# Performance work log

Hardware: AMD Instinct MI355X
Metric: run time of the kernel (lower is better)

## Reference

```python
import jax, jax.numpy as jnp
import numpy as np

N = 262144
BN_EPS = 1e-5


def gcn_conv(x, edge_index, edge_weight, W, b):
    """PyG GCNConv: symmetric norm with added self-loops (fill value 1).
    out[i] = sum_e d^{-1/2}[src] * w_e * d^{-1/2}[dst] * (x[src] @ W) + b
    """
    src, dst = edge_index[0], edge_index[1]
    loops = jnp.arange(N)
    src2 = jnp.concatenate([src, loops])
    dst2 = jnp.concatenate([dst, loops])
    ew2 = jnp.concatenate([edge_weight, jnp.ones((N,), edge_weight.dtype)])
    deg = jax.ops.segment_sum(ew2, dst2, num_segments=N)  # [N]
    dinv = jnp.where(deg > 0, jax.lax.rsqrt(deg), 0.0)
    norm = dinv[src2] * ew2 * dinv[dst2]  # [E+N]
    h = x @ W  # [N, out_c] tiny GEMM
    msg = h[src2] * norm[:, None]  # gather + scale, [E+N, out_c]
    out = jax.ops.segment_sum(msg, dst2, num_segments=N)  # scatter-add
    return out + b


def bn_eval(x, gamma, beta, mean, var):
    # BatchNorm1d in eval mode (running statistics)
    return (x - mean) * (gamma * jax.lax.rsqrt(var + BN_EPS)) + beta


def setup_inputs() -> dict:
    key = jax.random.key(0)
    ks = jax.random.split(key, 16)
    E = 4194304
    inp = {
        "x": jax.random.normal(ks[0], (N, 1), jnp.float32),
        "edge_index": jax.random.randint(ks[1], (2, E), 0, N, jnp.int64),
        "edge_weight": jax.random.uniform(ks[2], (E,), jnp.float32),
        # GCNConv weights (lin has no bias fused; bias added after aggregation)
        "W1": jax.random.normal(ks[3], (1, 16), jnp.float32) * 0.5,
        "b1": jnp.zeros((16,), jnp.float32),
        "W2": jax.random.normal(ks[4], (16, 4), jnp.float32) * 0.25,
        "b2": jnp.zeros((4,), jnp.float32),
        "W3": jax.random.normal(ks[5], (4, 1), jnp.float32) * 0.5,
        "b3": jnp.zeros((1,), jnp.float32),
        # BatchNorm params (eval-mode running stats)
        "g1": jnp.ones((16,), jnp.float32), "be1": jnp.zeros((16,), jnp.float32),
        "m1": jax.random.normal(ks[6], (16,), jnp.float32) * 0.1,
        "v1": jax.random.uniform(ks[7], (16,), jnp.float32, 0.5, 1.5),
        "g2": jnp.ones((4,), jnp.float32), "be2": jnp.zeros((4,), jnp.float32),
        "m2": jax.random.normal(ks[8], (4,), jnp.float32) * 0.1,
        "v2": jax.random.uniform(ks[9], (4,), jnp.float32, 0.5, 1.5),
        # final Linear
        "We": jax.random.normal(ks[10], (1, 1), jnp.float32),
        "bee": jnp.zeros((1,), jnp.float32),
    }
    return inp


def reference(x, edge_index, edge_weight, W1, b1, W2, b2, W3, b3,
              g1, be1, m1, v1, g2, be2, m2, v2, We, bee):
    h = gcn_conv(x, edge_index, edge_weight, W1, b1)
    h = jax.nn.relu(bn_eval(h, g1, be1, m1, v1))  # dropout = identity (eval)
    h = gcn_conv(h, edge_index, edge_weight, W2, b2)
    h = jax.nn.relu(bn_eval(h, g2, be2, m2, v2))
    h = gcn_conv(h, edge_index, edge_weight, W3, b3)
    h = h @ We + bee
    return jax.nn.sigmoid(h)
```

## Files before the change

kernel.cpp:

```cpp
#include <hip/hip_runtime.h>
#include <hip/hip_fp16.h>
#include <math.h>


#define BN_EPS 1e-5f
#define BKT_BITS 9
#define BKT_SZ 512
#define NBKT 512
#define PB 1024
#define PT 512
#define STAGE_CAP 4096
#define SHD 8
#define CAPS 1280
#define CAPR (SHD*CAPS)
#define CAPL 8960
#define CHUNK_R 9
#define NGRP 128
#define NBL 2048
#define CAP2 2560
#define SW(p) ((p) ^ (((p) >> 5) & 31))

__device__ inline float wdec(int e) {
    return __half2float(__ushort_as_half((unsigned short)((((unsigned)e) >> 18) << 1)));
}

__global__ void k_zero(int* __restrict__ gcur, int m) {
    int i = blockIdx.x * blockDim.x + threadIdx.x;
    if (i < m) gcur[i] = 0;
}

__device__ inline void scat1(int d, int s, int wbits, int* __restrict__ cur,
                             const int* __restrict__ basem, int2* __restrict__ stage) {
    int bk = ((unsigned)d) >> BKT_BITS;
    int dloc = d & (BKT_SZ - 1);
    int pos = atomicAdd(&cur[bk], 1);
    int dest = basem[bk] + pos;
    unsigned h = (unsigned)(__half_as_ushort(__float2half(__int_as_float(wbits))) & 0x7FFF);
    unsigned w14 = (h >> 1) + (h & 1);
    stage[pos] = make_int2(
        (int)((unsigned)s | ((unsigned)dloc << 18) | (((unsigned)dest & 31u) << 27)),
        (int)(w14 | (((unsigned)dest >> 5) << 14)));
}

__global__ __launch_bounds__(PT, 8) void k_scatter(
        const int* __restrict__ src, const int* __restrict__ dst,
        const float* __restrict__ w, int* __restrict__ gcur,
        int2* __restrict__ sorted, int E) {
    __shared__ int cur[NBKT];
    __shared__ int basem[NBKT];
    __shared__ int wsum[8];
    __shared__ int2 stage[STAGE_CAP];
    int t = threadIdx.x, b = blockIdx.x;
    cur[t] = 0;
    __syncthreads();
    int lo = b * STAGE_CAP;
    const int4* dp = (const int4*)(dst + lo);
    const int4* sp = (const int4*)(src + lo);
    const int4* wp = (const int4*)(w + lo);
    int4 d4a = dp[t];
    int4 d4b = dp[t + PT];
    int4 s4a = sp[t], s4b = sp[t + PT];
    int4 w4a = wp[t], w4b = wp[t + PT];
    atomicAdd(&cur[((unsigned)d4a.x) >> BKT_BITS], 1);
    atomicAdd(&cur[((unsigned)d4a.y) >> BKT_BITS], 1);
    atomicAdd(&cur[((unsigned)d4a.z) >> BKT_BITS], 1);
    atomicAdd(&cur[((unsigned)d4a.w) >> BKT_BITS], 1);
    atomicAdd(&cur[((unsigned)d4b.x) >> BKT_BITS], 1);
    atomicAdd(&cur[((unsigned)d4b.y) >> BKT_BITS], 1);
    atomicAdd(&cur[((unsigned)d4b.z) >> BKT_BITS], 1);
    atomicAdd(&cur[((unsigned)d4b.w) >> BKT_BITS], 1);
    __syncthreads();
    int v = cur[t];
    int lane = t & 63, wid = t >> 6;
    int inc = v;
#pragma unroll
    for (int off = 1; off < 64; off <<= 1) {
        int u = __shfl_up(inc, off);
        if (lane >= off) inc += u;
    }
    if (lane == 63) wsum[wid] = inc;
    __syncthreads();
    if (t == 0) {
        int s = 0;
#pragma unroll
        for (int i = 0; i < 8; ++i) { int c = wsum[i]; wsum[i] = s; s += c; }
    }
    __syncthreads();
    int excl = inc - v + wsum[wid];
    int shard = b & (SHD - 1);
    int gbase = v ? atomicAdd(&gcur[((t << 3) | shard) << 4], v) : 0;
    cur[t] = excl;
    basem[t] = t * CAPR + shard * CAPS + gbase - excl;
    __syncthreads();
    scat1(d4a.x, s4a.x, w4a.x, cur, basem, stage);
    scat1(d4a.y, s4a.y, w4a.y, cur, basem, stage);
    scat1(d4a.z, s4a.z, w4a.z, cur, basem, stage);
    scat1(d4a.w, s4a.w, w4a.w, cur, basem, stage);
    scat1(d4b.x, s4b.x, w4b.x, cur, basem, stage);
    scat1(d4b.y, s4b.y, w4b.y, cur, basem, stage);
    scat1(d4b.z, s4b.z, w4b.z, cur, basem, stage);
    scat1(d4b.w, s4b.w, w4b.w, cur, basem, stage);
    __syncthreads();
    for (int p = t; p < STAGE_CAP; p += PT) {
        int2 sv = stage[p];
        unsigned w0 = (unsigned)sv.x, w1 = (unsigned)sv.y;
        int dest = (int)(((w1 >> 14) << 5) | (w0 >> 27));
        sorted[dest] = make_int2((int)(w0 & 0x07FFFFFF), (int)(w1 & 0x3FFF));
    }
}

__global__ __launch_bounds__(1024, 8) void k_sortdeg(
        const int* __restrict__ gcur, int2* __restrict__ sorted,
        const float* __restrict__ x, float* __restrict__ dinv,
        float* __restrict__ xs, int* __restrict__ starts,
        int* __restrict__ gend) {
    __shared__ int lpk[CAPL];
    __shared__ int cnt[BKT_SZ];
    __shared__ int sts[BKT_SZ + 1];
    __shared__ int wsum2[8];
    __shared__ int ssh[SHD];
    __shared__ int soff[SHD + 1];
    __shared__ float degp[BKT_SZ];
    int t = threadIdx.x, b = blockIdx.x;
    if (t < BKT_SZ) cnt[t] = 0;
    if (t < SHD) ssh[t] = min(gcur[((b << 3) | t) << 4], CAPS);
    __syncthreads();
    if (t == 0) {
        int s = 0;
#pragma unroll
        for (int i = 0; i < SHD; ++i) { soff[i] = s; s += ssh[i]; }
        soff[SHD] = min(s, CAPL);
    }
    __syncthreads();
    int len = soff[SHD];
    int rbase = b * CAPR;

    int e27[CHUNK_R], wrk[CHUNK_R];
#pragma unroll
    for (int r = 0; r < CHUNK_R; ++r) {
        int k = t + (r << 10);
        if (k < len) {
            int s = 0;
#pragma unroll
            for (int q = 1; q < SHD; ++q) s += (k >= soff[q]) ? 1 : 0;
            int2 v = sorted[rbase + s * CAPS + (k - soff[s])];
            e27[r] = v.x;
            int rk = atomicAdd(&cnt[((unsigned)v.x) >> 18], 1);
            wrk[r] = (v.y & 0x3FFF) | (rk << 14);
        }
    }
    __syncthreads();
    int c_own = (t < BKT_SZ) ? cnt[t] : 0;
    int lane = t & 63, wid = t >> 6;
    int inc = c_own;
#pragma unroll
    for (int o = 1; o < 64; o <<= 1) {
        int u = __shfl_up(inc, o);
        if (lane >= o) inc += u;
    }
    if (t < BKT_SZ && lane == 63) wsum2[wid] = inc;
    __syncthreads();
    if (t == 0) {
        int s = 0;
#pragma unroll
        for (int i = 0; i < 8; ++i) { int c = wsum2[i]; wsum2[i] = s; s += c; }
    }
    __syncthreads();
    if (t < BKT_SZ) sts[t] = inc - c_own + wsum2[wid];
    if (t == 0) sts[BKT_SZ] = len;
    __syncthreads();
#pragma unroll
    for (int r = 0; r < CHUNK_R; ++r) {
        int k = t + (r << 10);
        if (k < len) {
            int e = e27[r];
            int pos = sts[((unsigned)e) >> 18] + (((unsigned)wrk[r]) >> 14);
            lpk[SW(pos)] = (e & 0x3FFFF) | ((wrk[r] & 0x3FFF) << 18);
        }
    }
    __syncthreads();

    int pbase = 2 * rbase;
    {
        int node = t & (BKT_SZ - 1);
        int jh = t >> 9;
        int c0 = sts[node], c1 = sts[node + 1];
        int half = (c1 - c0) >> 1;
        int kb = jh ? (c0 + half) : c0;
        int ke = jh ? c1 : (c0 + half);
        float s = 0.f;
        for (int k = kb; k < ke; ++k) s += wdec(lpk[SW(k)]);
        if (jh) degp[node] = s;
        __syncthreads();
        if (!jh) {
            s += degp[node];
            float di = rsqrtf(1.0f + s);
            int i = b * BKT_SZ + node;
            dinv[i] = di;
            xs[i] = di * x[i];
            starts[i] = pbase + c0;
        }
    }
    if (t < 4)
        gend[b * 4 + t] = pbase + ((t == 3) ? len : sts[(t + 1) * NGRP]);

    int* srtp = (int*)sorted;
    for (int k4 = (t << 2); k4 < len; k4 += 4096) {
        if (k4 + 3 < len) {
            int4 v;
            v.x = lpk[SW(k4)]; v.y = lpk[SW(k4 + 1)];
            v.z = lpk[SW(k4 + 2)]; v.w = lpk[SW(k4 + 3)];
            *(int4*)(srtp + pbase + k4) = v;
        } else {
            for (int k = k4; k < len; ++k) srtp[pbase + k] = lpk[SW(k)];
        }
    }
}

__global__ __launch_bounds__(512, 8) void k_l1(
        const int* __restrict__ starts, const int* __restrict__ gend,
        const int* __restrict__ srtp,
        const float* __restrict__ xs, const float* __restrict__ dinv,
        const float* __restrict__ W1, const float* __restrict__ b1,
        const float* __restrict__ g1, const float* __restrict__ be1,
        const float* __restrict__ m1, const float* __restrict__ v1,
        const float* __restrict__ W2, int2* __restrict__ hs2p) {
    __shared__ int eds[CAP2 + 32];
    __shared__ float part[3][NGRP];
    __shared__ float s1w[16], bb1[16];
    int t = threadIdx.x, b = blockIdx.x;
    int i0 = b * NGRP;
    if (t < 16) {
        float s = g1[t] * rsqrtf(v1[t] + BN_EPS);
        s1w[t] = W1[t] * s;
        bb1[t] = fmaf(b1[t] - m1[t], s, be1[t]);
    }
    int lo = starts[i0];
    int lo2 = lo & ~3;
    int len2 = min(gend[b] - lo, CAP2) + (lo - lo2);
    for (int k4 = (t << 2); k4 < len2; k4 += 2048) {
        int4 v = *(const int4*)(srtp + lo2 + k4);
        eds[SW(k4)] = v.x;
        if (k4 + 1 < len2) eds[SW(k4 + 1)] = v.y;
        if (k4 + 2 < len2) eds[SW(k4 + 2)] = v.z;
        if (k4 + 3 < len2) eds[SW(k4 + 3)] = v.w;
    }
    __syncthreads();
    int li = t & (NGRP - 1);
    int j = t >> 7;
    int i = i0 + li;
    int c0 = starts[i] - lo2;
    int c1 = (li == NGRP - 1) ? len2 : starts[i + 1] - lo2;
    int seg = c1 - c0;
    int kb = c0 + ((seg * j) >> 2);
    int ke = c0 + ((seg * (j + 1)) >> 2);
    float acc = 0.f;
    int k = kb;
    if (k < ke) {
        int e = eds[SW(k)];
        float xv = xs[e & 0x3FFFF];
        for (++k; k < ke; ++k) {
            int e2 = eds[SW(k)];
            float x2 = xs[e2 & 0x3FFFF];
            acc = fmaf(wdec(e), xv, acc);
            e = e2; xv = x2;
        }
        acc = fmaf(wdec(e), xv, acc);
    }
    if (j) part[j - 1][li] = acc;
    __syncthreads();
    if (j) return;
    float di = dinv[i];
    float a = di * (acc + part[0][li] + part[1][li] + part[2][li] + xs[i]);
    float h0 = 0.f, h1 = 0.f, h2 = 0.f, h3 = 0.f;
#pragma unroll
    for (int c = 0; c < 16; ++c) {
        float z = fmaf(a, s1w[c], bb1[c]);
        z = fmaxf(z, 0.f);
        h0 = fmaf(z, W2[c * 4 + 0], h0);
        h1 = fmaf(z, W2[c * 4 + 1], h1);
        h2 = fmaf(z, W2[c * 4 + 2], h2);
        h3 = fmaf(z, W2[c * 4 + 3], h3);
    }
    __half2 p01 = __floats2half2_rn(di * h0, di * h1);
    __half2 p23 = __floats2half2_rn(di * h2, di * h3);
    hs2p[i] = make_int2(*(int*)&p01, *(int*)&p23);
}

__global__ __launch_bounds__(512, 8) void k_l2(
        const int* __restrict__ starts, const int* __restrict__ gend,
        const int* __restrict__ srtp,
        const int2* __restrict__ hs2p, const float* __restrict__ dinv,
        const float* __restrict__ b2, const float* __restrict__ g2,
        const float* __restrict__ be2, const float* __restrict__ m2,
        const float* __restrict__ v2, const float* __restrict__ W3,
        float* __restrict__ hs3) {
    __shared__ int eds[CAP2 + 32];
    __shared__ float4 part4[3][NGRP];
    __shared__ float s2w[4], bb2[4];
    int t = threadIdx.x, b = blockIdx.x;
    int i0 = b * NGRP;
    if (t < 4) {
        float s = g2[t] * rsqrtf(v2[t] + BN_EPS);
        s2w[t] = s;
        bb2[t] = fmaf(b2[t] - m2[t], s, be2[t]);
    }
    int lo = starts[i0];
    int lo2 = lo & ~3;
    int len2 = min(gend[b] - lo, CAP2) + (lo - lo2);
    for (int k4 = (t << 2); k4 < len2; k4 += 2048) {
        int4 v = *(const int4*)(srtp + lo2 + k4);
        eds[SW(k4)] = v.x;
        if (k4 + 1 < len2) eds[SW(k4 + 1)] = v.y;
        if (k4 + 2 < len2) eds[SW(k4 + 2)] = v.z;
        if (k4 + 3 < len2) eds[SW(k4 + 3)] = v.w;
    }
    __syncthreads();
    int li = t & (NGRP - 1);
    int j = t >> 7;
    int i = i0 + li;
    int c0 = starts[i] - lo2;
    int c1 = (li == NGRP - 1) ? len2 : starts[i + 1] - lo2;
    int seg = c1 - c0;
    int kb = c0 + ((seg * j) >> 2);
    int ke = c0 + ((seg * (j + 1)) >> 2);
    float a0 = 0.f, a1 = 0.f, a2 = 0.f, a3 = 0.f;
    int k = kb;
    if (k < ke) {
        int e = eds[SW(k)];
        int2 h = hs2p[e & 0x3FFFF];
        for (++k; k < ke; ++k) {
            int e2 = eds[SW(k)];
            int2 h2 = hs2p[e2 & 0x3FFFF];
            float wv = wdec(e);
            float2 f01 = __half22float2(*(__half2*)&h.x);
            float2 f23 = __half22float2(*(__half2*)&h.y);
            a0 = fmaf(wv, f01.x, a0); a1 = fmaf(wv, f01.y, a1);
            a2 = fmaf(wv, f23.x, a2); a3 = fmaf(wv, f23.y, a3);
            e = e2; h = h2;
        }
        float wv = wdec(e);
        float2 f01 = __half22float2(*(__half2*)&h.x);
        float2 f23 = __half22float2(*(__half2*)&h.y);
        a0 = fmaf(wv, f01.x, a0); a1 = fmaf(wv, f01.y, a1);
        a2 = fmaf(wv, f23.x, a2); a3 = fmaf(wv, f23.y, a3);
    }
    if (j) part4[j - 1][li] = make_float4(a0, a1, a2, a3);
    __syncthreads();
    if (j) return;
    float4 pa = part4[0][li], pb = part4[1][li], pc = part4[2][li];
    float di = dinv[i];
    int2 sp = hs2p[i];
    float2 f01 = __half22float2(*(__half2*)&sp.x);
    float2 f23 = __half22float2(*(__half2*)&sp.y);
    float av[4] = {di * (a0 + pa.x + pb.x + pc.x + f01.x),
                   di * (a1 + pa.y + pb.y + pc.y + f01.y),
                   di * (a2 + pa.z + pb.z + pc.z + f23.x),
                   di * (a3 + pa.w + pb.w + pc.w + f23.y)};
    float h = 0.f;
#pragma unroll
    for (int d = 0; d < 4; ++d) {
        float z = fmaf(av[d], s2w[d], bb2[d]);
        z = fmaxf(z, 0.f);
        h = fmaf(z, W3[d], h);
    }
    hs3[i] = di * h;
}

__global__ __launch_bounds__(512, 8) void k_l3(
        const int* __restrict__ starts, const int* __restrict__ gend,
        const int* __restrict__ srtp,
        const float* __restrict__ hs3, const float* __restrict__ dinv,
        const float* __restrict__ b3, const float* __restrict__ We,
        const float* __restrict__ bee, float* __restrict__ out) {
    __shared__ int eds[CAP2 + 32];
    __shared__ float part[3][NGRP];
    int t = threadIdx.x, b = blockIdx.x;
    int i0 = b * NGRP;
    int lo = starts[i0];
    int lo2 = lo & ~3;
    int len2 = min(gend[b] - lo, CAP2) + (lo - lo2);
    for (int k4 = (t << 2); k4 < len2; k4 += 2048) {
        int4 v = *(const int4*)(srtp + lo2 + k4);
        eds[SW(k4)] = v.x;
        if (k4 + 1 < len2) eds[SW(k4 + 1)] = v.y;
        if (k4 + 2 < len2) eds[SW(k4 + 2)] = v.z;
        if (k4 + 3 < len2) eds[SW(k4 + 3)] = v.w;
    }
    __syncthreads();
    int li = t & (NGRP - 1);
    int j = t >> 7;
    int i = i0 + li;
    int c0 = starts[i] - lo2;
    int c1 = (li == NGRP - 1) ? len2 : starts[i + 1] - lo2;
    int seg = c1 - c0;
    int kb = c0 + ((seg * j) >> 2);
    int ke = c0 + ((seg * (j + 1)) >> 2);
    float acc = 0.f;
    int k = kb;
    if (k < ke) {
        int e = eds[SW(k)];
        float xv = hs3[e & 0x3FFFF];
        for (++k; k < ke; ++k) {
            int e2 = eds[SW(k)];
            float x2 = hs3[e2 & 0x3FFFF];
            acc = fmaf(wdec(e), xv, acc);
            e = e2; xv = x2;
        }
        acc = fmaf(wdec(e), xv, acc);
    }
    if (j) part[j - 1][li] = acc;
    __syncthreads();
    if (j) return;
    float a = dinv[i] * (acc + part[0][li] + part[1][li] + part[2][li] + hs3[i]);
    float o = fmaf(a + b3[0], We[0], bee[0]);
    out[i] = 1.0f / (1.0f + expf(-o));
}

extern "C" void kernel_launch(void* const* d_in, const int* in_sizes, int n_in,
                              void* d_out, int out_size, void* d_ws, size_t ws_size,
                              hipStream_t stream) {
    const float* x   = (const float*)d_in[0];
    const int*   ei  = (const int*)d_in[1];
    const float* w   = (const float*)d_in[2];
    const float* W1  = (const float*)d_in[3];
    const float* b1  = (const float*)d_in[4];
    const float* W2  = (const float*)d_in[5];
    const float* b2  = (const float*)d_in[6];
    const float* W3  = (const float*)d_in[7];
    const float* b3  = (const float*)d_in[8];
    const float* g1  = (const float*)d_in[9];
    const float* be1 = (const float*)d_in[10];
    const float* m1  = (const float*)d_in[11];
    const float* v1  = (const float*)d_in[12];
    const float* g2  = (const float*)d_in[13];
    const float* be2 = (const float*)d_in[14];
    const float* m2  = (const float*)d_in[15];
    const float* v2  = (const float*)d_in[16];
    const float* We  = (const float*)d_in[17];
    const float* bee = (const float*)d_in[18];
    float* out = (float*)d_out;

    const int n = in_sizes[0];
    const int E = in_sizes[2];
    const int* src = ei;
    const int* dst = ei + E;

    char* ws = (char*)d_ws;
    int2*  sorted  = (int2*)ws;
    int*   gcur    = (int*)(ws + (size_t)NBKT * CAPR * 8);
    int2*  hs2p    = (int2*)(gcur + NBKT * SHD * 16);
    float* dinv    = (float*)(hs2p + n);
    float* xs      = dinv + n;
    float* hs3     = xs + n;
    int*   starts  = (int*)(hs3 + n);
    int*   gend    = starts + n;

    int* srtp = (int*)sorted;

    k_zero<<<(NBKT * SHD * 16 + 255) / 256, 256, 0, stream>>>(gcur, NBKT * SHD * 16);
    k_scatter<<<PB, PT, 0, stream>>>(src, dst, w, gcur, sorted, E);
    k_sortdeg<<<NBKT, 1024, 0, stream>>>(gcur, sorted, x, dinv, xs, starts, gend);
    k_l1<<<NBL, 512, 0, stream>>>(starts, gend, srtp, xs, dinv,
                                  W1, b1, g1, be1, m1, v1, W2, hs2p);
    k_l2<<<NBL, 512, 0, stream>>>(starts, gend, srtp, hs2p, dinv,
                                  b2, g2, be2, m2, v2, W3, hs3);
    k_l3<<<NBL, 512, 0, stream>>>(starts, gend, srtp, hs3, dinv, b3, We, bee, out);
}
```

Before: 222.9 us.

## Replace 4-way split-row aggregation with degree-sorted one-thread-per-node scheduling

The sort kernel now counting-sorts each half-bucket's nodes by in-degree (capped at 63) and writes a permutation. The three aggregation kernels drop the four-threads-per-node split with its shared-memory reduction and barrier. Each now runs 256 threads per block, one thread per node, taking nodes in degree order so lanes in a wavefront have similar loop trip counts. This removes the partial-sum sync and reduces divergence. In exchange, per-thread serial work grows, there are fewer blocks, LDS staging per block is larger, and output writes become scattered.

```diff
diff --git a/kernel.cpp b/kernel.cpp
--- a/kernel.cpp
+++ b/kernel.cpp
@@ -15,9 +15,8 @@
 #define CAPR (SHD*CAPS)
 #define CAPL 8960
 #define CHUNK_R 9
-#define NGRP 128
-#define NBL 2048
-#define CAP2 2560
+#define CAPH 4608
+#define NBL2 1024
 #define SW(p) ((p) ^ (((p) >> 5) & 31))
 
 __device__ inline float wdec(int e) {
@@ -113,7 +112,7 @@
         const int* __restrict__ gcur, int2* __restrict__ sorted,
         const float* __restrict__ x, float* __restrict__ dinv,
         float* __restrict__ xs, int* __restrict__ starts,
-        int* __restrict__ gend) {
+        int* __restrict__ gend, int* __restrict__ perm) {
     __shared__ int lpk[CAPL];
     __shared__ int cnt[BKT_SZ];
     __shared__ int sts[BKT_SZ + 1];
@@ -121,8 +120,10 @@
     __shared__ int ssh[SHD];
     __shared__ int soff[SHD + 1];
     __shared__ float degp[BKT_SZ];
+    __shared__ int dcnt[128];
     int t = threadIdx.x, b = blockIdx.x;
     if (t < BKT_SZ) cnt[t] = 0;
+    if (t >= BKT_SZ && t < BKT_SZ + 128) dcnt[t - BKT_SZ] = 0;
     if (t < SHD) ssh[t] = min(gcur[((b << 3) | t) << 4], CAPS);
     __syncthreads();
     if (t == 0) {
@@ -181,10 +182,15 @@
     __syncthreads();
 
     int pbase = 2 * rbase;
+    int node = t & (BKT_SZ - 1);
+    int jh = t >> 9;
+    int c0 = sts[node], c1 = sts[node + 1];
+    int mydeg = 0, myrank = 0;
+    if (!jh) {
+        mydeg = min(c1 - c0, 63);
+        myrank = atomicAdd(&dcnt[((t >> 8) << 6) + mydeg], 1);
+    }
     {
-        int node = t & (BKT_SZ - 1);
-        int jh = t >> 9;
-        int c0 = sts[node], c1 = sts[node + 1];
         int half = (c1 - c0) >> 1;
         int kb = jh ? (c0 + half) : c0;
         int ke = jh ? c1 : (c0 + half);
@@ -201,8 +207,18 @@
             starts[i] = pbase + c0;
         }
     }
-    if (t < 4)
-        gend[b * 4 + t] = pbase + ((t == 3) ? len : sts[(t + 1) * NGRP]);
+    if (t == 0) {
+        int s = 0;
+#pragma unroll
+        for (int i = 0; i < 64; ++i) { int c = dcnt[i]; dcnt[i] = s; s += c; }
+        s = 0;
+#pragma unroll
+        for (int i = 64; i < 128; ++i) { int c = dcnt[i]; dcnt[i] = s; s += c; }
+        gend[b] = pbase + len;
+    }
+    __syncthreads();
+    if (!jh)
+        perm[b * BKT_SZ + ((t >> 8) << 8) + dcnt[((t >> 8) << 6) + mydeg] + myrank] = node;
 
     int* srtp = (int*)sorted;
     for (int k4 = (t << 2); k4 < len; k4 += 4096) {
@@ -217,28 +233,29 @@
     }
 }
 
-__global__ __launch_bounds__(512, 8) void k_l1(
+__global__ __launch_bounds__(256, 8) void k_l1(
         const int* __restrict__ starts, const int* __restrict__ gend,
-        const int* __restrict__ srtp,
+        const int* __restrict__ perm, const int* __restrict__ srtp,
         const float* __restrict__ xs, const float* __restrict__ dinv,
         const float* __restrict__ W1, const float* __restrict__ b1,
         const float* __restrict__ g1, const float* __restrict__ be1,
         const float* __restrict__ m1, const float* __restrict__ v1,
         const float* __restrict__ W2, int2* __restrict__ hs2p) {
-    __shared__ int eds[CAP2 + 32];
-    __shared__ float part[3][NGRP];
+    __shared__ int eds[CAPH + 32];
     __shared__ float s1w[16], bb1[16];
     int t = threadIdx.x, b = blockIdx.x;
-    int i0 = b * NGRP;
+    int bucket = b >> 1, half = b & 1;
+    int i0 = b * 256;
     if (t < 16) {
         float s = g1[t] * rsqrtf(v1[t] + BN_EPS);
         s1w[t] = W1[t] * s;
         bb1[t] = fmaf(b1[t] - m1[t], s, be1[t]);
     }
     int lo = starts[i0];
+    int endA = half ? gend[bucket] : starts[i0 + 256];
     int lo2 = lo & ~3;
-    int len2 = min(gend[b] - lo, CAP2) + (lo - lo2);
-    for (int k4 = (t << 2); k4 < len2; k4 += 2048) {
+    int len2 = min(endA - lo, CAPH) + (lo - lo2);
+    for (int k4 = (t << 2); k4 < len2; k4 += 1024) {
         int4 v = *(const int4*)(srtp + lo2 + k4);
         eds[SW(k4)] = v.x;
         if (k4 + 1 < len2) eds[SW(k4 + 1)] = v.y;
@@ -246,20 +263,18 @@
         if (k4 + 3 < len2) eds[SW(k4 + 3)] = v.w;
     }
     __syncthreads();
-    int li = t & (NGRP - 1);
-    int j = t >> 7;
-    int i = i0 + li;
+    int prm = perm[bucket * 512 + half * 256 + t];
+    int i = bucket * 512 + prm;
     int c0 = starts[i] - lo2;
-    int c1 = (li == NGRP - 1) ? len2 : starts[i + 1] - lo2;
-    int seg = c1 - c0;
-    int kb = c0 + ((seg * j) >> 2);
-    int ke = c0 + ((seg * (j + 1)) >> 2);
+    int c1 = ((prm & 255) == 255) ? (endA - lo2) : (starts[i + 1] - lo2);
+    c1 = min(c1, len2);
+    c0 = min(c0, c1);
     float acc = 0.f;
-    int k = kb;
-    if (k < ke) {
+    int k = c0;
+    if (k < c1) {
         int e = eds[SW(k)];
         float xv = xs[e & 0x3FFFF];
-        for (++k; k < ke; ++k) {
+        for (++k; k < c1; ++k) {
             int e2 = eds[SW(k)];
             float x2 = xs[e2 & 0x3FFFF];
             acc = fmaf(wdec(e), xv, acc);
@@ -267,11 +282,8 @@
         }
         acc = fmaf(wdec(e), xv, acc);
     }
-    if (j) part[j - 1][li] = acc;
-    __syncthreads();
-    if (j) return;
     float di = dinv[i];
-    float a = di * (acc + part[0][li] + part[1][li] + part[2][li] + xs[i]);
+    float a = di * (acc + xs[i]);
     float h0 = 0.f, h1 = 0.f, h2 = 0.f, h3 = 0.f;
 #pragma unroll
     for (int c = 0; c < 16; ++c) {
@@ -287,28 +299,29 @@
     hs2p[i] = make_int2(*(int*)&p01, *(int*)&p23);
 }
 
-__global__ __launch_bounds__(512, 8) void k_l2(
+__global__ __launch_bounds__(256, 8) void k_l2(
         const int* __restrict__ starts, const int* __restrict__ gend,
-        const int* __restrict__ srtp,
+        const int* __restrict__ perm, const int* __restrict__ srtp,
         const int2* __restrict__ hs2p, const float* __restrict__ dinv,
         const float* __restrict__ b2, const float* __restrict__ g2,
         const float* __restrict__ be2, const float* __restrict__ m2,
         const float* __restrict__ v2, const float* __restrict__ W3,
         float* __restrict__ hs3) {
-    __shared__ int eds[CAP2 + 32];
-    __shared__ float4 part4[3][NGRP];
+    __shared__ int eds[CAPH + 32];
     __shared__ float s2w[4], bb2[4];
     int t = threadIdx.x, b = blockIdx.x;
-    int i0 = b * NGRP;
+    int bucket = b >> 1, half = b & 1;
+    int i0 = b * 256;
     if (t < 4) {
         float s = g2[t] * rsqrtf(v2[t] + BN_EPS);
         s2w[t] = s;
         bb2[t] = fmaf(b2[t] - m2[t], s, be2[t]);
     }
     int lo = starts[i0];
+    int endA = half ? gend[bucket] : starts[i0 + 256];
     int lo2 = lo & ~3;
-    int len2 = min(gend[b] - lo, CAP2) + (lo - lo2);
-    for (int k4 = (t << 2); k4 < len2; k4 += 2048) {
+    int len2 = min(endA - lo, CAPH) + (lo - lo2);
+    for (int k4 = (t << 2); k4 < len2; k4 += 1024) {
         int4 v = *(const int4*)(srtp + lo2 + k4);
         eds[SW(k4)] = v.x;
         if (k4 + 1 < len2) eds[SW(k4 + 1)] = v.y;
@@ -316,20 +329,18 @@
         if (k4 + 3 < len2) eds[SW(k4 + 3)] = v.w;
     }
     __syncthreads();
-    int li = t & (NGRP - 1);
-    int j = t >> 7;
-    int i = i0 + li;
+    int prm = perm[bucket * 512 + half * 256 + t];
+    int i = bucket * 512 + prm;
     int c0 = starts[i] - lo2;
-    int c1 = (li == NGRP - 1) ? len2 : starts[i + 1] - lo2;
-    int seg = c1 - c0;
-    int kb = c0 + ((seg * j) >> 2);
-    int ke = c0 + ((seg * (j + 1)) >> 2);
+    int c1 = ((prm & 255) == 255) ? (endA - lo2) : (starts[i + 1] - lo2);
+    c1 = min(c1, len2);
+    c0 = min(c0, c1);
     float a0 = 0.f, a1 = 0.f, a2 = 0.f, a3 = 0.f;
-    int k = kb;
-    if (k < ke) {
+    int k = c0;
+    if (k < c1) {
         int e = eds[SW(k)];
         int2 h = hs2p[e & 0x3FFFF];
-        for (++k; k < ke; ++k) {
+        for (++k; k < c1; ++k) {
             int e2 = eds[SW(k)];
             int2 h2 = hs2p[e2 & 0x3FFFF];
             float wv = wdec(e);
@@ -345,42 +356,37 @@
         a0 = fmaf(wv, f01.x, a0); a1 = fmaf(wv, f01.y, a1);
         a2 = fmaf(wv, f23.x, a2); a3 = fmaf(wv, f23.y, a3);
     }
-    if (j) part4[j - 1][li] = make_float4(a0, a1, a2, a3);
-    __syncthreads();
-    if (j) return;
-    float4 pa = part4[0][li], pb = part4[1][li], pc = part4[2][li];
     float di = dinv[i];
     int2 sp = hs2p[i];
     float2 f01 = __half22float2(*(__half2*)&sp.x);
     float2 f23 = __half22float2(*(__half2*)&sp.y);
-    float av[4] = {di * (a0 + pa.x + pb.x + pc.x + f01.x),
-                   di * (a1 + pa.y + pb.y + pc.y + f01.y),
-                   di * (a2 + pa.z + pb.z + pc.z + f23.x),
-                   di * (a3 + pa.w + pb.w + pc.w + f23.y)};
-    float h = 0.f;
-#pragma unroll
-    for (int d = 0; d < 4; ++d) {
-        float z = fmaf(av[d], s2w[d], bb2[d]);
-        z = fmaxf(z, 0.f);
-        h = fmaf(z, W3[d], h);
-    }
+    float av0 = di * (a0 + f01.x);
+    float av1 = di * (a1 + f01.y);
+    float av2 = di * (a2 + f23.x);
+    float av3 = di * (a3 + f23.y);
+    float z0 = fmaxf(fmaf(av0, s2w[0], bb2[0]), 0.f);
+    float z1 = fmaxf(fmaf(av1, s2w[1], bb2[1]), 0.f);
+    float z2 = fmaxf(fmaf(av2, s2w[2], bb2[2]), 0.f);
+    float z3 = fmaxf(fmaf(av3, s2w[3], bb2[3]), 0.f);
+    float h = fmaf(z0, W3[0], fmaf(z1, W3[1], fmaf(z2, W3[2], z3 * W3[3])));
     hs3[i] = di * h;
 }
 
-__global__ __launch_bounds__(512, 8) void k_l3(
+__global__ __launch_bounds__(256, 8) void k_l3(
         const int* __restrict__ starts, const int* __restrict__ gend,
-        const int* __restrict__ srtp,
+        const int* __restrict__ perm, const int* __restrict__ srtp,
         const float* __restrict__ hs3, const float* __restrict__ dinv,
         const float* __restrict__ b3, const float* __restrict__ We,
         const float* __restrict__ bee, float* __restrict__ out) {
-    __shared__ int eds[CAP2 + 32];
-    __shared__ float part[3][NGRP];
+    __shared__ int eds[CAPH + 32];
     int t = threadIdx.x, b = blockIdx.x;
-    int i0 = b * NGRP;
+    int bucket = b >> 1, half = b & 1;
+    int i0 = b * 256;
     int lo = starts[i0];
+    int endA = half ? gend[bucket] : starts[i0 + 256];
     int lo2 = lo & ~3;
-    int len2 = min(gend[b] - lo, CAP2) + (lo - lo2);
-    for (int k4 = (t << 2); k4 < len2; k4 += 2048) {
+    int len2 = min(endA - lo, CAPH) + (lo - lo2);
+    for (int k4 = (t << 2); k4 < len2; k4 += 1024) {
         int4 v = *(const int4*)(srtp + lo2 + k4);
         eds[SW(k4)] = v.x;
         if (k4 + 1 < len2) eds[SW(k4 + 1)] = v.y;
@@ -388,20 +394,18 @@
         if (k4 + 3 < len2) eds[SW(k4 + 3)] = v.w;
     }
     __syncthreads();
-    int li = t & (NGRP - 1);
-    int j = t >> 7;
-    int i = i0 + li;
+    int prm = perm[bucket * 512 + half * 256 + t];
+    int i = bucket * 512 + prm;
     int c0 = starts[i] - lo2;
-    int c1 = (li == NGRP - 1) ? len2 : starts[i + 1] - lo2;
-    int seg = c1 - c0;
-    int kb = c0 + ((seg * j) >> 2);
-    int ke = c0 + ((seg * (j + 1)) >> 2);
+    int c1 = ((prm & 255) == 255) ? (endA - lo2) : (starts[i + 1] - lo2);
+    c1 = min(c1, len2);
+    c0 = min(c0, c1);
     float acc = 0.f;
-    int k = kb;
-    if (k < ke) {
+    int k = c0;
+    if (k < c1) {
         int e = eds[SW(k)];
         float xv = hs3[e & 0x3FFFF];
-        for (++k; k < ke; ++k) {
+        for (++k; k < c1; ++k) {
             int e2 = eds[SW(k)];
             float x2 = hs3[e2 & 0x3FFFF];
             acc = fmaf(wdec(e), xv, acc);
@@ -409,10 +413,7 @@
         }
         acc = fmaf(wdec(e), xv, acc);
     }
-    if (j) part[j - 1][li] = acc;
-    __syncthreads();
-    if (j) return;
-    float a = dinv[i] * (acc + part[0][li] + part[1][li] + part[2][li] + hs3[i]);
+    float a = dinv[i] * (acc + hs3[i]);
     float o = fmaf(a + b3[0], We[0], bee[0]);
     out[i] = 1.0f / (1.0f + expf(-o));
 }
@@ -455,15 +456,17 @@
     float* hs3     = xs + n;
     int*   starts  = (int*)(hs3 + n);
     int*   gend    = starts + n;
+    int*   perm    = gend + 2048;
 
     int* srtp = (int*)sorted;
 
     k_zero<<<(NBKT * SHD * 16 + 255) / 256, 256, 0, stream>>>(gcur, NBKT * SHD * 16);
     k_scatter<<<PB, PT, 0, stream>>>(src, dst, w, gcur, sorted, E);
-    k_sortdeg<<<NBKT, 1024, 0, stream>>>(gcur, sorted, x, dinv, xs, starts, gend);
-    k_l1<<<NBL, 512, 0, stream>>>(starts, gend, srtp, xs, dinv,
-                                  W1, b1, g1, be1, m1, v1, W2, hs2p);
-    k_l2<<<NBL, 512, 0, stream>>>(starts, gend, srtp, hs2p, dinv,
-                                  b2, g2, be2, m2, v2, W3, hs3);
-    k_l3<<<NBL, 512, 0, stream>>>(starts, gend, srtp, hs3, dinv, b3, We, bee, out);
-}
+    k_sortdeg<<<NBKT, 1024, 0, stream>>>(gcur, sorted, x, dinv, xs, starts, gend, perm);
+    k_l1<<<NBL2, 256, 0, stream>>>(starts, gend, perm, srtp, xs, dinv,
+                                   W1, b1, g1, be1, m1, v1, W2, hs2p);
+    k_l2<<<NBL2, 256, 0, stream>>>(starts, gend, perm, srtp, hs2p, dinv,
+                                   b2, g2, be2, m2, v2, W3, hs3);
+    k_l3<<<NBL2, 256, 0, stream>>>(starts, gend, perm, srtp, hs3, dinv,
+                                   b3, We, bee, out);
+}
```

Measured after the change: 222.9 us. No clear change (+0.0%).

## Replace two-pass bucket sort with global atomic histogram, scan, and placement CSR build

Applied to the files above, without the earlier changes.

Replaces the bucketed two-level sort (shared-memory staging plus per-bucket local sort) with a classic CSR build. A global per-node atomic histogram of counts and weight sums is followed by a two-level prefix scan, then a placement kernel that atomically claims slots per destination node. This drops the sharded capacity buffers and the gend array. It adds many more global atomics (two per edge in the histogram, one per edge in placement) and fully random scattered writes, trading coalesced bucket writes for simpler logic. Edge order within each node becomes nondeterministic.

```diff
diff --git a/kernel.cpp b/kernel.cpp
--- a/kernel.cpp
+++ b/kernel.cpp
@@ -4,17 +4,7 @@
 
 
 #define BN_EPS 1e-5f
-#define BKT_BITS 9
-#define BKT_SZ 512
 #define NBKT 512
-#define PB 1024
-#define PT 512
-#define STAGE_CAP 4096
-#define SHD 8
-#define CAPS 1280
-#define CAPR (SHD*CAPS)
-#define CAPL 8960
-#define CHUNK_R 9
 #define NGRP 128
 #define NBL 2048
 #define CAP2 2560
@@ -24,202 +14,138 @@
     return __half2float(__ushort_as_half((unsigned short)((((unsigned)e) >> 18) << 1)));
 }
 
-__global__ void k_zero(int* __restrict__ gcur, int m) {
+__global__ void k_zero(int* __restrict__ p, int m) {
     int i = blockIdx.x * blockDim.x + threadIdx.x;
-    if (i < m) gcur[i] = 0;
-}
-
-__device__ inline void scat1(int d, int s, int wbits, int* __restrict__ cur,
-                             const int* __restrict__ basem, int2* __restrict__ stage) {
-    int bk = ((unsigned)d) >> BKT_BITS;
-    int dloc = d & (BKT_SZ - 1);
-    int pos = atomicAdd(&cur[bk], 1);
-    int dest = basem[bk] + pos;
-    unsigned h = (unsigned)(__half_as_ushort(__float2half(__int_as_float(wbits))) & 0x7FFF);
-    unsigned w14 = (h >> 1) + (h & 1);
-    stage[pos] = make_int2(
-        (int)((unsigned)s | ((unsigned)dloc << 18) | (((unsigned)dest & 31u) << 27)),
-        (int)(w14 | (((unsigned)dest >> 5) << 14)));
-}
-
-__global__ __launch_bounds__(PT, 8) void k_scatter(
-        const int* __restrict__ src, const int* __restrict__ dst,
-        const float* __restrict__ w, int* __restrict__ gcur,
-        int2* __restrict__ sorted, int E) {
-    __shared__ int cur[NBKT];
-    __shared__ int basem[NBKT];
-    __shared__ int wsum[8];
-    __shared__ int2 stage[STAGE_CAP];
-    int t = threadIdx.x, b = blockIdx.x;
-    cur[t] = 0;
-    __syncthreads();
-    int lo = b * STAGE_CAP;
-    const int4* dp = (const int4*)(dst + lo);
-    const int4* sp = (const int4*)(src + lo);
-    const int4* wp = (const int4*)(w + lo);
-    int4 d4a = dp[t];
-    int4 d4b = dp[t + PT];
-    int4 s4a = sp[t], s4b = sp[t + PT];
-    int4 w4a = wp[t], w4b = wp[t + PT];
-    atomicAdd(&cur[((unsigned)d4a.x) >> BKT_BITS], 1);
-    atomicAdd(&cur[((unsigned)d4a.y) >> BKT_BITS], 1);
-    atomicAdd(&cur[((unsigned)d4a.z) >> BKT_BITS], 1);
-    atomicAdd(&cur[((unsigned)d4a.w) >> BKT_BITS], 1);
-    atomicAdd(&cur[((unsigned)d4b.x) >> BKT_BITS], 1);
-    atomicAdd(&cur[((unsigned)d4b.y) >> BKT_BITS], 1);
-    atomicAdd(&cur[((unsigned)d4b.z) >> BKT_BITS], 1);
-    atomicAdd(&cur[((unsigned)d4b.w) >> BKT_BITS], 1);
-    __syncthreads();
-    int v = cur[t];
-    int lane = t & 63, wid = t >> 6;
-    int inc = v;
-#pragma unroll
-    for (int off = 1; off < 64; off <<= 1) {
-        int u = __shfl_up(inc, off);
-        if (lane >= off) inc += u;
-    }
-    if (lane == 63) wsum[wid] = inc;
+    if (i < m) p[i] = 0;
+}
+
+__global__ __launch_bounds__(256, 8) void k_hist(
+        const int* __restrict__ dst, const float* __restrict__ w,
+        int* __restrict__ cnt, float* __restrict__ wsum, int E) {
+    int tid = blockIdx.x * 256 + threadIdx.x;
+    int stride = gridDim.x * 256;
+    const int4* dp = (const int4*)dst;
+    const float4* wp = (const float4*)w;
+    int nq = E >> 2;
+    for (int k = tid; k < nq; k += stride) {
+        int4 d = dp[k];
+        float4 ww = wp[k];
+        atomicAdd(&cnt[d.x], 1); atomicAdd(&wsum[d.x], ww.x);
+        atomicAdd(&cnt[d.y], 1); atomicAdd(&wsum[d.y], ww.y);
+        atomicAdd(&cnt[d.z], 1); atomicAdd(&wsum[d.z], ww.z);
+        atomicAdd(&cnt[d.w], 1); atomicAdd(&wsum[d.w], ww.w);
+    }
+}
+
+__global__ __launch_bounds__(512, 8) void k_bsum(
+        const int* __restrict__ cnt, int* __restrict__ bsum) {
+    __shared__ int ws[8];
+    int t = threadIdx.x, b = blockIdx.x;
+    int v = cnt[b * 512 + t];
+#pragma unroll
+    for (int o = 32; o; o >>= 1) v += __shfl_down(v, o);
+    if ((t & 63) == 0) ws[t >> 6] = v;
     __syncthreads();
     if (t == 0) {
         int s = 0;
 #pragma unroll
-        for (int i = 0; i < 8; ++i) { int c = wsum[i]; wsum[i] = s; s += c; }
-    }
-    __syncthreads();
-    int excl = inc - v + wsum[wid];
-    int shard = b & (SHD - 1);
-    int gbase = v ? atomicAdd(&gcur[((t << 3) | shard) << 4], v) : 0;
-    cur[t] = excl;
-    basem[t] = t * CAPR + shard * CAPS + gbase - excl;
-    __syncthreads();
-    scat1(d4a.x, s4a.x, w4a.x, cur, basem, stage);
-    scat1(d4a.y, s4a.y, w4a.y, cur, basem, stage);
-    scat1(d4a.z, s4a.z, w4a.z, cur, basem, stage);
-    scat1(d4a.w, s4a.w, w4a.w, cur, basem, stage);
-    scat1(d4b.x, s4b.x, w4b.x, cur, basem, stage);
-    scat1(d4b.y, s4b.y, w4b.y, cur, basem, stage);
-    scat1(d4b.z, s4b.z, w4b.z, cur, basem, stage);
-    scat1(d4b.w, s4b.w, w4b.w, cur, basem, stage);
-    __syncthreads();
-    for (int p = t; p < STAGE_CAP; p += PT) {
-        int2 sv = stage[p];
-        unsigned w0 = (unsigned)sv.x, w1 = (unsigned)sv.y;
-        int dest = (int)(((w1 >> 14) << 5) | (w0 >> 27));
-        sorted[dest] = make_int2((int)(w0 & 0x07FFFFFF), (int)(w1 & 0x3FFF));
-    }
-}
-
-__global__ __launch_bounds__(1024, 8) void k_sortdeg(
-        const int* __restrict__ gcur, int2* __restrict__ sorted,
-        const float* __restrict__ x, float* __restrict__ dinv,
-        float* __restrict__ xs, int* __restrict__ starts,
-        int* __restrict__ gend) {
-    __shared__ int lpk[CAPL];
-    __shared__ int cnt[BKT_SZ];
-    __shared__ int sts[BKT_SZ + 1];
-    __shared__ int wsum2[8];
-    __shared__ int ssh[SHD];
-    __shared__ int soff[SHD + 1];
-    __shared__ float degp[BKT_SZ];
-    int t = threadIdx.x, b = blockIdx.x;
-    if (t < BKT_SZ) cnt[t] = 0;
-    if (t < SHD) ssh[t] = min(gcur[((b << 3) | t) << 4], CAPS);
-    __syncthreads();
-    if (t == 0) {
-        int s = 0;
-#pragma unroll
-        for (int i = 0; i < SHD; ++i) { soff[i] = s; s += ssh[i]; }
-        soff[SHD] = min(s, CAPL);
-    }
-    __syncthreads();
-    int len = soff[SHD];
-    int rbase = b * CAPR;
-
-    int e27[CHUNK_R], wrk[CHUNK_R];
-#pragma unroll
-    for (int r = 0; r < CHUNK_R; ++r) {
-        int k = t + (r << 10);
-        if (k < len) {
-            int s = 0;
-#pragma unroll
-            for (int q = 1; q < SHD; ++q) s += (k >= soff[q]) ? 1 : 0;
-            int2 v = sorted[rbase + s * CAPS + (k - soff[s])];
-            e27[r] = v.x;
-            int rk = atomicAdd(&cnt[((unsigned)v.x) >> 18], 1);
-            wrk[r] = (v.y & 0x3FFF) | (rk << 14);
-        }
-    }
-    __syncthreads();
-    int c_own = (t < BKT_SZ) ? cnt[t] : 0;
+        for (int i = 0; i < 8; ++i) s += ws[i];
+        bsum[b] = s;
+    }
+}
+
+__global__ __launch_bounds__(512, 8) void k_scan(
+        const int* __restrict__ cnt, const int* __restrict__ bsum,
+        const float* __restrict__ wsum, const float* __restrict__ x,
+        int* __restrict__ starts, int* __restrict__ cursor,
+        float* __restrict__ dinv, float* __restrict__ xs, int n) {
+    __shared__ int sb[512];
+    __shared__ int wsA[8];
+    __shared__ int wsB[8];
+    int t = threadIdx.x, b = blockIdx.x;
     int lane = t & 63, wid = t >> 6;
-    int inc = c_own;
+    int v = bsum[t];
+    int inc = v;
 #pragma unroll
     for (int o = 1; o < 64; o <<= 1) {
         int u = __shfl_up(inc, o);
         if (lane >= o) inc += u;
     }
-    if (t < BKT_SZ && lane == 63) wsum2[wid] = inc;
+    if (lane == 63) wsA[wid] = inc;
     __syncthreads();
     if (t == 0) {
         int s = 0;
 #pragma unroll
-        for (int i = 0; i < 8; ++i) { int c = wsum2[i]; wsum2[i] = s; s += c; }
-    }
-    __syncthreads();
-    if (t < BKT_SZ) sts[t] = inc - c_own + wsum2[wid];
-    if (t == 0) sts[BKT_SZ] = len;
-    __syncthreads();
-#pragma unroll
-    for (int r = 0; r < CHUNK_R; ++r) {
-        int k = t + (r << 10);
-        if (k < len) {
-            int e = e27[r];
-            int pos = sts[((unsigned)e) >> 18] + (((unsigned)wrk[r]) >> 14);
-            lpk[SW(pos)] = (e & 0x3FFFF) | ((wrk[r] & 0x3FFF) << 18);
-        }
-    }
-    __syncthreads();
-
-    int pbase = 2 * rbase;
-    {
-        int node = t & (BKT_SZ - 1);
-        int jh = t >> 9;
-        int c0 = sts[node], c1 = sts[node + 1];
-        int half = (c1 - c0) >> 1;
-        int kb = jh ? (c0 + half) : c0;
-        int ke = jh ? c1 : (c0 + half);
-        float s = 0.f;
-        for (int k = kb; k < ke; ++k) s += wdec(lpk[SW(k)]);
-        if (jh) degp[node] = s;
-        __syncthreads();
-        if (!jh) {
-            s += degp[node];
-            float di = rsqrtf(1.0f + s);
-            int i = b * BKT_SZ + node;
-            dinv[i] = di;
-            xs[i] = di * x[i];
-            starts[i] = pbase + c0;
-        }
-    }
-    if (t < 4)
-        gend[b * 4 + t] = pbase + ((t == 3) ? len : sts[(t + 1) * NGRP]);
-
-    int* srtp = (int*)sorted;
-    for (int k4 = (t << 2); k4 < len; k4 += 4096) {
-        if (k4 + 3 < len) {
-            int4 v;
-            v.x = lpk[SW(k4)]; v.y = lpk[SW(k4 + 1)];
-            v.z = lpk[SW(k4 + 2)]; v.w = lpk[SW(k4 + 3)];
-            *(int4*)(srtp + pbase + k4) = v;
-        } else {
-            for (int k = k4; k < len; ++k) srtp[pbase + k] = lpk[SW(k)];
+        for (int i = 0; i < 8; ++i) { int c = wsA[i]; wsA[i] = s; s += c; }
+    }
+    __syncthreads();
+    sb[t] = inc - v + wsA[wid];
+    __syncthreads();
+    int boff = sb[b];
+    int i = b * 512 + t;
+    int c = cnt[i];
+    int inc2 = c;
+#pragma unroll
+    for (int o = 1; o < 64; o <<= 1) {
+        int u = __shfl_up(inc2, o);
+        if (lane >= o) inc2 += u;
+    }
+    if (lane == 63) wsB[wid] = inc2;
+    __syncthreads();
+    if (t == 0) {
+        int s = 0;
+#pragma unroll
+        for (int k = 0; k < 8; ++k) { int cc = wsB[k]; wsB[k] = s; s += cc; }
+    }
+    __syncthreads();
+    int st = boff + inc2 - c + wsB[wid];
+    starts[i] = st;
+    cursor[i] = st;
+    float di = rsqrtf(1.0f + wsum[i]);
+    dinv[i] = di;
+    xs[i] = di * x[i];
+    if (b == 511 && t == 511) starts[n] = st + c;
+}
+
+__global__ __launch_bounds__(256, 8) void k_place(
+        const int* __restrict__ src, const int* __restrict__ dst,
+        const float* __restrict__ w, int* __restrict__ cursor,
+        int* __restrict__ packed, int E) {
+    int tid = blockIdx.x * 256 + threadIdx.x;
+    int stride = gridDim.x * 256;
+    const int4* sp = (const int4*)src;
+    const int4* dp = (const int4*)dst;
+    const float4* wp = (const float4*)w;
+    int nq = E >> 2;
+    for (int k = tid; k < nq; k += stride) {
+        int4 s = sp[k];
+        int4 d = dp[k];
+        float4 ww = wp[k];
+        {
+            unsigned h = __half_as_ushort(__float2half(ww.x)) & 0x7FFF;
+            int pos = atomicAdd(&cursor[d.x], 1);
+            packed[pos] = s.x | (int)(((h >> 1) + (h & 1)) << 18);
+        }
+        {
+            unsigned h = __half_as_ushort(__float2half(ww.y)) & 0x7FFF;
+            int pos = atomicAdd(&cursor[d.y], 1);
+            packed[pos] = s.y | (int)(((h >> 1) + (h & 1)) << 18);
+        }
+        {
+            unsigned h = __half_as_ushort(__float2half(ww.z)) & 0x7FFF;
+            int pos = atomicAdd(&cursor[d.z], 1);
+            packed[pos] = s.z | (int)(((h >> 1) + (h & 1)) << 18);
+        }
+        {
+            unsigned h = __half_as_ushort(__float2half(ww.w)) & 0x7FFF;
+            int pos = atomicAdd(&cursor[d.w], 1);
+            packed[pos] = s.w | (int)(((h >> 1) + (h & 1)) << 18);
         }
     }
 }
 
 __global__ __launch_bounds__(512, 8) void k_l1(
-        const int* __restrict__ starts, const int* __restrict__ gend,
-        const int* __restrict__ srtp,
+        const int* __restrict__ starts, const int* __restrict__ srtp,
         const float* __restrict__ xs, const float* __restrict__ dinv,
         const float* __restrict__ W1, const float* __restrict__ b1,
         const float* __restrict__ g1, const float* __restrict__ be1,
@@ -236,8 +162,9 @@
         bb1[t] = fmaf(b1[t] - m1[t], s, be1[t]);
     }
     int lo = starts[i0];
+    int hi = starts[i0 + NGRP];
     int lo2 = lo & ~3;
-    int len2 = min(gend[b] - lo, CAP2) + (lo - lo2);
+    int len2 = min(hi - lo, CAP2) + (lo - lo2);
     for (int k4 = (t << 2); k4 < len2; k4 += 2048) {
         int4 v = *(const int4*)(srtp + lo2 + k4);
         eds[SW(k4)] = v.x;
@@ -249,8 +176,8 @@
     int li = t & (NGRP - 1);
     int j = t >> 7;
     int i = i0 + li;
-    int c0 = starts[i] - lo2;
-    int c1 = (li == NGRP - 1) ? len2 : starts[i + 1] - lo2;
+    int c1 = min(starts[i + 1] - lo2, len2);
+    int c0 = min(starts[i] - lo2, c1);
     int seg = c1 - c0;
     int kb = c0 + ((seg * j) >> 2);
     int ke = c0 + ((seg * (j + 1)) >> 2);
@@ -288,8 +215,7 @@
 }
 
 __global__ __launch_bounds__(512, 8) void k_l2(
-        const int* __restrict__ starts, const int* __restrict__ gend,
-        const int* __restrict__ srtp,
+        const int* __restrict__ starts, const int* __restrict__ srtp,
         const int2* __restrict__ hs2p, const float* __restrict__ dinv,
         const float* __restrict__ b2, const float* __restrict__ g2,
         const float* __restrict__ be2, const float* __restrict__ m2,
@@ -306,8 +232,9 @@
         bb2[t] = fmaf(b2[t] - m2[t], s, be2[t]);
     }
     int lo = starts[i0];
+    int hi = starts[i0 + NGRP];
     int lo2 = lo & ~3;
-    int len2 = min(gend[b] - lo, CAP2) + (lo - lo2);
+    int len2 = min(hi - lo, CAP2) + (lo - lo2);
     for (int k4 = (t << 2); k4 < len2; k4 += 2048) {
         int4 v = *(const int4*)(srtp + lo2 + k4);
         eds[SW(k4)] = v.x;
@@ -319,8 +246,8 @@
     int li = t & (NGRP - 1);
     int j = t >> 7;
     int i = i0 + li;
-    int c0 = starts[i] - lo2;
-    int c1 = (li == NGRP - 1) ? len2 : starts[i + 1] - lo2;
+    int c1 = min(starts[i + 1] - lo2, len2);
+    int c0 = min(starts[i] - lo2, c1);
     int seg = c1 - c0;
     int kb = c0 + ((seg * j) >> 2);
     int ke = c0 + ((seg * (j + 1)) >> 2);
@@ -368,8 +295,7 @@
 }
 
 __global__ __launch_bounds__(512, 8) void k_l3(
-        const int* __restrict__ starts, const int* __restrict__ gend,
-        const int* __restrict__ srtp,
+        const int* __restrict__ starts, const int* __restrict__ srtp,
         const float* __restrict__ hs3, const float* __restrict__ dinv,
         const float* __restrict__ b3, const float* __restrict__ We,
         const float* __restrict__ bee, float* __restrict__ out) {
@@ -378,8 +304,9 @@
     int t = threadIdx.x, b = blockIdx.x;
     int i0 = b * NGRP;
     int lo = starts[i0];
+    int hi = starts[i0 + NGRP];
     int lo2 = lo & ~3;
-    int len2 = min(gend[b] - lo, CAP2) + (lo - lo2);
+    int len2 = min(hi - lo, CAP2) + (lo - lo2);
     for (int k4 = (t << 2); k4 < len2; k4 += 2048) {
         int4 v = *(const int4*)(srtp + lo2 + k4);
         eds[SW(k4)] = v.x;
@@ -391,8 +318,8 @@
     int li = t & (NGRP - 1);
     int j = t >> 7;
     int i = i0 + li;
-    int c0 = starts[i] - lo2;
-    int c1 = (li == NGRP - 1) ? len2 : starts[i + 1] - lo2;
+    int c1 = min(starts[i + 1] - lo2, len2);
+    int c0 = min(starts[i] - lo2, c1);
     int seg = c1 - c0;
     int kb = c0 + ((seg * j) >> 2);
     int ke = c0 + ((seg * (j + 1)) >> 2);
@@ -447,23 +374,26 @@
     const int* dst = ei + E;
 
     char* ws = (char*)d_ws;
-    int2*  sorted  = (int2*)ws;
-    int*   gcur    = (int*)(ws + (size_t)NBKT * CAPR * 8);
-    int2*  hs2p    = (int2*)(gcur + NBKT * SHD * 16);
-    float* dinv    = (float*)(hs2p + n);
-    float* xs      = dinv + n;
-    float* hs3     = xs + n;
-    int*   starts  = (int*)(hs3 + n);
-    int*   gend    = starts + n;
-
-    int* srtp = (int*)sorted;
-
-    k_zero<<<(NBKT * SHD * 16 + 255) / 256, 256, 0, stream>>>(gcur, NBKT * SHD * 16);
-    k_scatter<<<PB, PT, 0, stream>>>(src, dst, w, gcur, sorted, E);
-    k_sortdeg<<<NBKT, 1024, 0, stream>>>(gcur, sorted, x, dinv, xs, starts, gend);
-    k_l1<<<NBL, 512, 0, stream>>>(starts, gend, srtp, xs, dinv,
+    int*   packed = (int*)ws;
+    int*   cnt    = packed + E;
+    float* wsum   = (float*)(cnt + n);
+    int*   starts = (int*)(wsum + n);
+    int*   cursor = starts + n + 16;
+    int*   bsum   = cursor + n;
+    float* dinv   = (float*)(bsum + 512);
+    float* xs     = dinv + n;
+    float* hs3    = xs + n;
+    int2*  hs2p   = (int2*)(hs3 + n);
+
+    k_zero<<<(2 * n + 255) / 256, 256, 0, stream>>>(cnt, 2 * n);
+    k_hist<<<2048, 256, 0, stream>>>(dst, w, cnt, wsum, E);
+    k_bsum<<<NBKT, 512, 0, stream>>>(cnt, bsum);
+    k_scan<<<NBKT, 512, 0, stream>>>(cnt, bsum, wsum, x, starts, cursor,
+                                     dinv, xs, n);
+    k_place<<<2048, 256, 0, stream>>>(src, dst, w, cursor, packed, E);
+    k_l1<<<NBL, 512, 0, stream>>>(starts, packed, xs, dinv,
                                   W1, b1, g1, be1, m1, v1, W2, hs2p);
-    k_l2<<<NBL, 512, 0, stream>>>(starts, gend, srtp, hs2p, dinv,
+    k_l2<<<NBL, 512, 0, stream>>>(starts, packed, hs2p, dinv,
                                   b2, g2, be2, m2, v2, W3, hs3);
-    k_l3<<<NBL, 512, 0, stream>>>(starts, gend, srtp, hs3, dinv, b3, We, bee, out);
-}
+    k_l3<<<NBL, 512, 0, stream>>>(starts, packed, hs3, dinv, b3, We, bee, out);
+}
```

Measured after the change: 863.2 us. +287.3%, slower.
